# Kernel optimization log

Hardware: AMD Instinct MI355X
Metric: run time of the kernel (lower is better)

Reference implementation:

```python
import jax, jax.numpy as jnp
import numpy as np

WINDOW = 20  # window_size from init

def setup_inputs() -> dict:
    key = jax.random.key(0)
    ks = jax.random.split(key, 8)
    B, K, L, H = 8, 64, 1024, 256
    FFN = 3 * H * 4  # input_dim*ffn_ratio
    cand_span_reps = jax.random.normal(ks[0], (B, K, H), dtype=jnp.float32)
    token_reps = jax.random.normal(ks[1], (B, L, H), dtype=jnp.float32)
    W1 = jax.random.normal(ks[2], (3 * H, FFN), dtype=jnp.float32) * (1.0 / np.sqrt(3 * H))
    b1 = jnp.zeros((FFN,), dtype=jnp.float32)
    W2 = jax.random.normal(ks[3], (FFN, H), dtype=jnp.float32) * (1.0 / np.sqrt(FFN))
    b2 = jnp.zeros((H,), dtype=jnp.float32)
    cand_span_ids = jnp.sort(jax.random.randint(ks[4], (B, K, 2), 0, L), axis=-1)
    token_masks = jnp.ones((B, L), dtype=bool)
    return {"cand_span_reps": cand_span_reps, "token_reps": token_reps,
            "W1": W1, "b1": b1, "W2": W2, "b2": b2,
            "cand_span_ids": cand_span_ids, "token_masks": token_masks}

def _span_window_max(token_reps, span_ids, token_masks, window):
    # token_reps: [B,L,H]; span_ids: [B,K,2]; token_masks: [B,L]
    L = token_reps.shape[1]
    seq = jnp.arange(L)[None, None, :]                      # [1,1,L]
    start = span_ids[:, :, 0][:, :, None]                   # [B,K,1]
    end = span_ids[:, :, 1][:, :, None]                     # [B,K,1]
    mask = (((seq >= start - window) & (seq < start)) |
            ((seq > end) & (seq <= end + window)))
    mask = mask & token_masks[:, None, :]                   # [B,K,L]
    # masked max over L -> [B,K,H]
    filled = jnp.where(mask[..., None], token_reps[:, None, :, :], -jnp.inf)
    return jnp.max(filled, axis=2)

def reference(cand_span_reps, token_reps, W1, b1, W2, b2, cand_span_ids, token_masks):
    B, K, H = cand_span_reps.shape
    # Per-span pooled window context [B,K,H]. The pairwise context over the
    # UNION of head & tail windows equals the elementwise max of the two
    # per-span window maxes (max over A|B == max(max A, max B)).
    ctx = _span_window_max(token_reps, cand_span_ids, token_masks, WINDOW)
    context_reps = jnp.maximum(ctx[:, :, None, :], ctx[:, None, :, :])   # [B,K,K,H]
    head_reps = jnp.broadcast_to(cand_span_reps[:, :, None, :], (B, K, K, H))
    tail_reps = jnp.broadcast_to(cand_span_reps[:, None, :, :], (B, K, K, H))
    rel = jnp.concatenate([head_reps, tail_reps, context_reps], axis=-1)  # [B,K,K,3H]
    h = jax.nn.relu(jnp.einsum('bijd,df->bijf', rel, W1) + b1)
    out = jnp.einsum('bijf,fh->bijh', h, W2) + b2
    return out.reshape(B, K * K, H)
```

## Files before the change

kernel.cpp:

```cpp
#include <hip/hip_runtime.h>
#include <hip/hip_bf16.h>
#include <cstdint>
#include <cstddef>


typedef __attribute__((ext_vector_type(8))) short short8;
typedef __attribute__((ext_vector_type(4))) float f32x4;
typedef __attribute__((ext_vector_type(2))) unsigned int u32x2;

#define B_DIM 8
#define K_DIM 64
#define H_DIM 256
#define L_DIM 1024
#define FFN_DIM 3072
#define WINDOW 20

__device__ __forceinline__ unsigned short f2b(float f) {
  unsigned int u = __float_as_uint(f);
  unsigned int r = (u + 0x7FFFu + ((u >> 16) & 1u)) >> 16;
  return (unsigned short)r;
}
__device__ __forceinline__ float b2f(unsigned short h) {
  return __uint_as_float(((unsigned int)h) << 16);
}
__device__ __forceinline__ f32x4 zero4() {
  f32x4 z = {0.f, 0.f, 0.f, 0.f};
  return z;
}
__device__ __forceinline__ void gload_lds16(const void* g, void* l) {
  __builtin_amdgcn_global_load_lds(
      (const __attribute__((address_space(1))) void*)g,
      (__attribute__((address_space(3))) void*)l, 16, 0, 0);
}
__device__ __forceinline__ unsigned int cvt_pk_bf16(float lo, float hi) {
  unsigned int r;
  asm("v_cvt_pk_bf16_f32 %0, %1, %2" : "=v"(r) : "v"(lo), "v"(hi));
  return r;
}


__global__ void cvt_bf16_kernel(const float* __restrict__ in,
                                unsigned short* __restrict__ out, int n) {
  int i = blockIdx.x * blockDim.x + threadIdx.x;
  if (i < n) out[i] = f2b(in[i]);
}

__global__ void transpose_cvt_kernel(const float* __restrict__ in,
                                     unsigned short* __restrict__ out,
                                     int R, int C) {
  __shared__ float t[64][65];
  int c0 = blockIdx.x * 64, r0 = blockIdx.y * 64;
  int tr = threadIdx.x >> 6, tc = threadIdx.x & 63;
  for (int rr = tr; rr < 64; rr += 4)
    t[rr][tc] = in[(size_t)(r0 + rr) * C + (c0 + tc)];
  __syncthreads();
  for (int cc = tr; cc < 64; cc += 4)
    out[(size_t)(c0 + cc) * R + (r0 + tc)] = f2b(t[tc][cc]);
}

__global__ void ctx_kernel(const float* __restrict__ token,
                           const int* __restrict__ ids,
                           unsigned short* __restrict__ ctx) {
  int bk = blockIdx.x;
  int b = bk >> 6;
  int h = threadIdx.x;
  int s = ids[bk * 2 + 0];
  int e = ids[bk * 2 + 1];
  const float* tb = token + ((size_t)b * L_DIM) * H_DIM + h;
  float m = -INFINITY;
  int lo = s - WINDOW; if (lo < 0) lo = 0;
  for (int l2 = lo; l2 < s; ++l2) m = fmaxf(m, tb[(size_t)l2 * H_DIM]);
  int hi = e + WINDOW; if (hi > L_DIM - 1) hi = L_DIM - 1;
  for (int l2 = e + 1; l2 <= hi; ++l2) m = fmaxf(m, tb[(size_t)l2 * H_DIM]);
  ctx[(size_t)bk * H_DIM + h] = f2b(m);
}

__global__ __launch_bounds__(256) void at_gemm_kernel(
    const unsigned short* __restrict__ candb,
    const unsigned short* __restrict__ w1abt,
    const float* __restrict__ b1, float* __restrict__ AT) {
  int n0 = blockIdx.x * 64;
  int r0 = blockIdx.y * 64;
  __shared__ __align__(16) unsigned short A[64 * 256];
  int w = threadIdx.x >> 6, l = threadIdx.x & 63;
  int l15 = l & 15, l4 = l >> 4;
  {
    int row = w * 16 + l15;
    const short8* src = (const short8*)(candb + (size_t)(r0 + row) * H_DIM);
    #pragma unroll
    for (int t = 0; t < 8; ++t) {
      int u = l4 + 4 * t;
      short8 v = src[u];
      *(short8*)(A + row * 256 + ((u ^ (row & 7)) * 8)) = v;
    }
  }
  __syncthreads();
  f32x4 acc[4] = {zero4(), zero4(), zero4(), zero4()};
  int n = n0 + 16 * w + l15;
  const unsigned short* bp = w1abt + (size_t)n * H_DIM + l4 * 8;
  #pragma unroll
  for (int kk = 0; kk < 8; ++kk) {
    short8 bfrag = *(const short8*)(bp + kk * 32);
    #pragma unroll
    for (int rf = 0; rf < 4; ++rf) {
      int row = rf * 16 + l15;
      int u = kk * 4 + l4;
      short8 afrag = *(const short8*)(A + row * 256 + ((u ^ (row & 7)) * 8));
      acc[rf] = __builtin_amdgcn_mfma_f32_16x16x32_bf16(afrag, bfrag, acc[rf], 0, 0, 0);
    }
  }
  float bias = (n < FFN_DIM) ? b1[n] : 0.0f;
  #pragma unroll
  for (int rf = 0; rf < 4; ++rf) {
    #pragma unroll
    for (int qq = 0; qq < 4; ++qq) {
      int row = r0 + rf * 16 + l4 * 4 + qq;
      AT[(size_t)row * (2 * FFN_DIM) + n] = acc[rf][qq] + bias;
    }
  }
}

__global__ __launch_bounds__(512, 4) void fused_kernel(
    const unsigned short* __restrict__ ctx,
    const unsigned short* __restrict__ w1ct,
    const unsigned short* __restrict__ w2t,
    const float* __restrict__ AT,
    const float* __restrict__ b2,
    float* __restrict__ out) {
  int blk = blockIdx.x;
  blk = (blk & 7) * 64 + (blk >> 3);
  int b = blk >> 6, i = blk & 63;

  __shared__ __align__(16) char W1s[2 * 16384];
  __shared__ __align__(16) char W2s[2 * 16384];
  __shared__ __align__(16) char HcS[2 * 4096];

  int tid = threadIdx.x;
  int w = tid >> 6, l = tid & 63;
  int l15 = l & 15, l4 = l >> 4;
  int wl = l15 & 7;
  int s3 = (l15 >> 1) & 3;

  if (w < 4) {
    int wf = w & 1, wj2 = w >> 1;
    int jloc = 32 * wj2 + l15;

    short8 bfr[8][2];
    {
      const unsigned short* cb = ctx + ((size_t)b * K_DIM) * H_DIM;
      const unsigned short* ci = cb + (size_t)i * H_DIM;
      #pragma unroll
      for (int kk = 0; kk < 8; ++kk) {
        int hoff = kk * 32 + l4 * 8;
        short8 vi = *(const short8*)(ci + hoff);
        #pragma unroll
        for (int jb = 0; jb < 2; ++jb) {
          short8 vj = *(const short8*)(cb + (size_t)(jloc + jb * 16) * H_DIM + hoff);
          short8 vm;
          #pragma unroll
          for (int e = 0; e < 8; ++e) {
            float fa = b2f((unsigned short)vi[e]);
            float fb = b2f((unsigned short)vj[e]);
            vm[e] = (fa >= fb) ? vi[e] : vj[e];
          }
          bfr[kk][jb] = vm;
        }
      }
    }

    int tid_p = (w << 6) | l;
    int fr = tid_p >> 5, u32i = tid_p & 31;
    int offW1 = fr * 512 + (((u32i & 24) | ((u32i & 7) ^ (fr & 7))) << 4);
    auto stageW1 = [&](int c, int buf) {
      const char* g = (const char*)w1ct + (size_t)c * 16384 + offW1;
      char* d = &W1s[buf * 16384 + tid_p * 16];
      gload_lds16(g, d);
      gload_lds16(g + 4096, d + 4096);
      gload_lds16(g + 8192, d + 8192);
      gload_lds16(g + 12288, d + 12288);
    };

    int baseA = (16 * wf + l15) * 512;
    int offAe = (l4 ^ wl) << 4;
    int offAo = ((4 + l4) ^ wl) << 4;
    int uW = 2 * wf + (l4 >> 1);
    int offHw = jloc * 64 + ((uW ^ s3) << 4) + ((l4 & 1) << 3);

    const float* avp = AT + (size_t)(b * K_DIM + i) * (2 * FFN_DIM) + 16 * wf + 4 * l4;
    const float* tvp = AT + (size_t)(b * K_DIM + jloc) * (2 * FFN_DIM) + FFN_DIM + 16 * wf + 4 * l4;

    stageW1(0, 0);
    __builtin_amdgcn_sched_barrier(0);
    asm volatile("s_waitcnt vmcnt(0)" ::: "memory");
    __builtin_amdgcn_sched_barrier(0);
    __builtin_amdgcn_s_barrier();
    __builtin_amdgcn_sched_barrier(0);

    for (int c = 0; c <= 96; ++c) {
      f32x4 av = zero4(), tv0 = zero4(), tv1 = zero4();
      if (c < 96) {
        av  = *(const f32x4*)(avp + c * 32);
        tv0 = *(const f32x4*)(tvp + c * 32);
        tv1 = *(const f32x4*)(tvp + 16 * (2 * FFN_DIM) + c * 32);
      }
      __builtin_amdgcn_sched_barrier(0);
      if (c < 95) stageW1(c + 1, (c + 1) & 1);
      __builtin_amdgcn_sched_barrier(0);

      if (c < 96) {
        const char* w1p = &W1s[(c & 1) * 16384 + baseA];
        f32x4 acc1[2] = {zero4(), zero4()};
        __builtin_amdgcn_s_setprio(1);
        #pragma unroll
        for (int m = 0; m < 4; ++m) {
          short8 afe = *(const short8*)(w1p + m * 128 + offAe);
          acc1[0] = __builtin_amdgcn_mfma_f32_16x16x32_bf16(afe, bfr[2 * m][0], acc1[0], 0, 0, 0);
          acc1[1] = __builtin_amdgcn_mfma_f32_16x16x32_bf16(afe, bfr[2 * m][1], acc1[1], 0, 0, 0);
          short8 afo = *(const short8*)(w1p + m * 128 + offAo);
          acc1[0] = __builtin_amdgcn_mfma_f32_16x16x32_bf16(afo, bfr[2 * m + 1][0], acc1[0], 0, 0, 0);
          acc1[1] = __builtin_amdgcn_mfma_f32_16x16x32_bf16(afo, bfr[2 * m + 1][1], acc1[1], 0, 0, 0);
        }
        __builtin_amdgcn_s_setprio(0);

        char* hw = &HcS[(c & 1) * 4096];
        {
          float v0 = fmaxf(acc1[0][0] + av[0] + tv0[0], 0.0f);
          float v1 = fmaxf(acc1[0][1] + av[1] + tv0[1], 0.0f);
          float v2 = fmaxf(acc1[0][2] + av[2] + tv0[2], 0.0f);
          float v3 = fmaxf(acc1[0][3] + av[3] + tv0[3], 0.0f);
          u32x2 pk;
          pk.x = cvt_pk_bf16(v0, v1);
          pk.y = cvt_pk_bf16(v2, v3);
          *(u32x2*)(hw + offHw) = pk;
        }
        {
          float v0 = fmaxf(acc1[1][0] + av[0] + tv1[0], 0.0f);
          float v1 = fmaxf(acc1[1][1] + av[1] + tv1[1], 0.0f);
          float v2 = fmaxf(acc1[1][2] + av[2] + tv1[2], 0.0f);
          float v3 = fmaxf(acc1[1][3] + av[3] + tv1[3], 0.0f);
          u32x2 pk;
          pk.x = cvt_pk_bf16(v0, v1);
          pk.y = cvt_pk_bf16(v2, v3);
          *(u32x2*)(hw + offHw + 1024) = pk;
        }
      }

      __builtin_amdgcn_sched_barrier(0);
      asm volatile("s_waitcnt vmcnt(0) lgkmcnt(0)" ::: "memory");
      __builtin_amdgcn_sched_barrier(0);
      __builtin_amdgcn_s_barrier();
      __builtin_amdgcn_sched_barrier(0);
    }
  } else {
    int ch = w - 4;
    int tid_c = (ch << 6) | l;
    int h2 = tid_c >> 2, u2 = tid_c & 3;
    int offW2 = h2 * 6144 + ((u2 ^ ((h2 >> 1) & 3)) << 4);
    auto stageW2 = [&](int c, int buf) {
      const char* g = (const char*)w2t + (size_t)c * 64 + offW2;
      char* d = &W2s[buf * 16384 + tid_c * 16];
      gload_lds16(g, d);
      gload_lds16(g + 1 * 393216, d + 4096);
      gload_lds16(g + 2 * 393216, d + 8192);
      gload_lds16(g + 3 * 393216, d + 12288);
    };
    int baseW2 = ch * 4096 + l15 * 64 + ((l4 ^ s3) << 4);
    int baseHr = l15 * 64 + ((l4 ^ s3) << 4);

    f32x4 accO[4][4];
    #pragma unroll
    for (int cf = 0; cf < 4; ++cf)
      #pragma unroll
      for (int jt = 0; jt < 4; ++jt) accO[cf][jt] = zero4();

    __builtin_amdgcn_s_barrier();
    __builtin_amdgcn_sched_barrier(0);

    for (int c = 0; c <= 96; ++c) {
      if (c < 96) stageW2(c, c & 1);
      __builtin_amdgcn_sched_barrier(0);

      if (c > 0) {
        const char* w2p = &W2s[((c - 1) & 1) * 16384];
        const char* hcp = &HcS[((c - 1) & 1) * 4096];
        short8 wfr[4], hbv[4];
        #pragma unroll
        for (int cf = 0; cf < 4; ++cf)
          wfr[cf] = *(const short8*)(w2p + baseW2 + cf * 1024);
        #pragma unroll
        for (int jt = 0; jt < 4; ++jt)
          hbv[jt] = *(const short8*)(hcp + baseHr + jt * 1024);
        __builtin_amdgcn_s_setprio(1);
        #pragma unroll
        for (int cf = 0; cf < 4; ++cf)
          #pragma unroll
          for (int jt = 0; jt < 4; ++jt)
            accO[cf][jt] = __builtin_amdgcn_mfma_f32_16x16x32_bf16(wfr[cf], hbv[jt], accO[cf][jt], 0, 0, 0);
        __builtin_amdgcn_s_setprio(0);
      }

      __builtin_amdgcn_sched_barrier(0);
      asm volatile("s_waitcnt vmcnt(0) lgkmcnt(0)" ::: "memory");
      __builtin_amdgcn_sched_barrier(0);
      __builtin_amdgcn_s_barrier();
      __builtin_amdgcn_sched_barrier(0);
    }

    f32x4 bv[4];
    #pragma unroll
    for (int cf = 0; cf < 4; ++cf)
      bv[cf] = *(const f32x4*)(b2 + 64 * ch + cf * 16 + 4 * l4);
    #pragma unroll
    for (int jt = 0; jt < 4; ++jt) {
      int j = jt * 16 + l15;
      float* row = out + ((size_t)b * (K_DIM * K_DIM) + (size_t)i * K_DIM + j) * H_DIM;
      #pragma unroll
      for (int cf = 0; cf < 4; ++cf) {
        f32x4 v = accO[cf][jt] + bv[cf];
        *(f32x4*)(row + 64 * ch + cf * 16 + 4 * l4) = v;
      }
    }
  }
}


extern "C" void kernel_launch(void* const* d_in, const int* in_sizes, int n_in,
                              void* d_out, int out_size, void* d_ws, size_t ws_size,
                              hipStream_t stream) {
  const float* cand  = (const float*)d_in[0];
  const float* token = (const float*)d_in[1];
  const float* W1    = (const float*)d_in[2];
  const float* b1    = (const float*)d_in[3];
  const float* W2    = (const float*)d_in[4];
  const float* b2    = (const float*)d_in[5];
  const int*   ids   = (const int*)d_in[6];
  float* out = (float*)d_out;

  char* ws = (char*)d_ws;
  unsigned short* ctx   = (unsigned short*)(ws);
  unsigned short* candb = (unsigned short*)(ws + 262144);
  unsigned short* w1abt = (unsigned short*)(ws + 524288);
  unsigned short* w1ct  = (unsigned short*)(ws + 3670016);
  unsigned short* w2t   = (unsigned short*)(ws + 5242880);
  float*          AT    = (float*)(ws + 6815744);

  hipLaunchKernelGGL(cvt_bf16_kernel, dim3(512), dim3(256), 0, stream,
                     cand, candb, B_DIM * K_DIM * H_DIM);
  hipLaunchKernelGGL(transpose_cvt_kernel, dim3(48, 4), dim3(256), 0, stream,
                     W1, w1abt, 256, FFN_DIM);
  hipLaunchKernelGGL(transpose_cvt_kernel, dim3(48, 4), dim3(256), 0, stream,
                     W1 + (size_t)256 * FFN_DIM, w1abt + (size_t)FFN_DIM * 256, 256, FFN_DIM);
  hipLaunchKernelGGL(transpose_cvt_kernel, dim3(48, 4), dim3(256), 0, stream,
                     W1 + (size_t)512 * FFN_DIM, w1ct, 256, FFN_DIM);
  hipLaunchKernelGGL(transpose_cvt_kernel, dim3(4, 48), dim3(256), 0, stream,
                     W2, w2t, FFN_DIM, 256);
  hipLaunchKernelGGL(ctx_kernel, dim3(512), dim3(256), 0, stream, token, ids, ctx);
  hipLaunchKernelGGL(at_gemm_kernel, dim3(96, 8), dim3(256), 0, stream,
                     candb, w1abt, b1, AT);
  hipLaunchKernelGGL(fused_kernel, dim3(512), dim3(512), 0, stream,
                     ctx, w1ct, w2t, AT, b2, out);
}
```

Measured before the change: 185.6 us.

## Move W1 tile staging from producer waves to consumer waves

The W1 global-to-LDS staging loads move out of the first-GEMM waves into the second-GEMM waves, which now issue both the W1 and W2 async copies each iteration. The producer waves keep only their small bias-vector loads and MFMA work. Address arithmetic is also switched to incremented pointers instead of per-iteration offset recomputation. The aim is to free the critical-path producer waves from memory-issue work, at the cost of loading more onto the consumer waves and making the W1 prefetch depend on their timing relative to the barrier.

New measurement: 181.2 us. 1.02x faster.

```diff
diff --git a/kernel.cpp b/kernel.cpp
--- a/kernel.cpp
+++ b/kernel.cpp
@@ -168,46 +168,27 @@
       }
     }
 
-    int tid_p = (w << 6) | l;
-    int fr = tid_p >> 5, u32i = tid_p & 31;
-    int offW1 = fr * 512 + (((u32i & 24) | ((u32i & 7) ^ (fr & 7))) << 4);
-    auto stageW1 = [&](int c, int buf) {
-      const char* g = (const char*)w1ct + (size_t)c * 16384 + offW1;
-      char* d = &W1s[buf * 16384 + tid_p * 16];
-      gload_lds16(g, d);
-      gload_lds16(g + 4096, d + 4096);
-      gload_lds16(g + 8192, d + 8192);
-      gload_lds16(g + 12288, d + 12288);
-    };
-
     int baseA = (16 * wf + l15) * 512;
     int offAe = (l4 ^ wl) << 4;
     int offAo = ((4 + l4) ^ wl) << 4;
     int uW = 2 * wf + (l4 >> 1);
     int offHw = jloc * 64 + ((uW ^ s3) << 4) + ((l4 & 1) << 3);
 
-    const float* avp = AT + (size_t)(b * K_DIM + i) * (2 * FFN_DIM) + 16 * wf + 4 * l4;
-    const float* tvp = AT + (size_t)(b * K_DIM + jloc) * (2 * FFN_DIM) + FFN_DIM + 16 * wf + 4 * l4;
-
-    stageW1(0, 0);
-    __builtin_amdgcn_sched_barrier(0);
-    asm volatile("s_waitcnt vmcnt(0)" ::: "memory");
-    __builtin_amdgcn_sched_barrier(0);
+    const float* avp  = AT + (size_t)(b * K_DIM + i) * (2 * FFN_DIM) + 16 * wf + 4 * l4;
+    const float* tvp0 = AT + (size_t)(b * K_DIM + jloc) * (2 * FFN_DIM) + FFN_DIM + 16 * wf + 4 * l4;
+    const float* tvp1 = tvp0 + (size_t)16 * (2 * FFN_DIM);
+
     __builtin_amdgcn_s_barrier();
     __builtin_amdgcn_sched_barrier(0);
 
     for (int c = 0; c <= 96; ++c) {
-      f32x4 av = zero4(), tv0 = zero4(), tv1 = zero4();
       if (c < 96) {
-        av  = *(const f32x4*)(avp + c * 32);
-        tv0 = *(const f32x4*)(tvp + c * 32);
-        tv1 = *(const f32x4*)(tvp + 16 * (2 * FFN_DIM) + c * 32);
-      }
-      __builtin_amdgcn_sched_barrier(0);
-      if (c < 95) stageW1(c + 1, (c + 1) & 1);
-      __builtin_amdgcn_sched_barrier(0);
-
-      if (c < 96) {
+        f32x4 av  = *(const f32x4*)avp;
+        f32x4 tv0 = *(const f32x4*)tvp0;
+        f32x4 tv1 = *(const f32x4*)tvp1;
+        avp += 32; tvp0 += 32; tvp1 += 32;
+        __builtin_amdgcn_sched_barrier(0);
+
         const char* w1p = &W1s[(c & 1) * 16384 + baseA];
         f32x4 acc1[2] = {zero4(), zero4()};
         __builtin_amdgcn_s_setprio(1);
@@ -254,16 +235,17 @@
   } else {
     int ch = w - 4;
     int tid_c = (ch << 6) | l;
+
+    int fr = tid_c >> 5, u32i = tid_c & 31;
+    int offW1 = fr * 512 + (((u32i & 24) | ((u32i & 7) ^ (fr & 7))) << 4);
     int h2 = tid_c >> 2, u2 = tid_c & 3;
     int offW2 = h2 * 6144 + ((u2 ^ ((h2 >> 1) & 3)) << 4);
-    auto stageW2 = [&](int c, int buf) {
-      const char* g = (const char*)w2t + (size_t)c * 64 + offW2;
-      char* d = &W2s[buf * 16384 + tid_c * 16];
-      gload_lds16(g, d);
-      gload_lds16(g + 1 * 393216, d + 4096);
-      gload_lds16(g + 2 * 393216, d + 8192);
-      gload_lds16(g + 3 * 393216, d + 12288);
-    };
+
+    const char* gW1 = (const char*)w1ct + offW1;
+    const char* gW2 = (const char*)w2t + offW2;
+    char* dW1base = &W1s[tid_c * 16];
+    char* dW2base = &W2s[tid_c * 16];
+
     int baseW2 = ch * 4096 + l15 * 64 + ((l4 ^ s3) << 4);
     int baseHr = l15 * 64 + ((l4 ^ s3) << 4);
 
@@ -273,11 +255,36 @@
       #pragma unroll
       for (int jt = 0; jt < 4; ++jt) accO[cf][jt] = zero4();
 
+    {
+      gload_lds16(gW1, dW1base);
+      gload_lds16(gW1 + 4096, dW1base + 4096);
+      gload_lds16(gW1 + 8192, dW1base + 8192);
+      gload_lds16(gW1 + 12288, dW1base + 12288);
+      gW1 += 16384;
+    }
+    __builtin_amdgcn_sched_barrier(0);
+    asm volatile("s_waitcnt vmcnt(0)" ::: "memory");
+    __builtin_amdgcn_sched_barrier(0);
     __builtin_amdgcn_s_barrier();
     __builtin_amdgcn_sched_barrier(0);
 
     for (int c = 0; c <= 96; ++c) {
-      if (c < 96) stageW2(c, c & 1);
+      if (c < 95) {
+        char* d = dW1base + ((c + 1) & 1) * 16384;
+        gload_lds16(gW1, d);
+        gload_lds16(gW1 + 4096, d + 4096);
+        gload_lds16(gW1 + 8192, d + 8192);
+        gload_lds16(gW1 + 12288, d + 12288);
+        gW1 += 16384;
+      }
+      if (c < 96) {
+        char* d = dW2base + (c & 1) * 16384;
+        gload_lds16(gW2, d);
+        gload_lds16(gW2 + 1 * 393216, d + 4096);
+        gload_lds16(gW2 + 2 * 393216, d + 8192);
+        gload_lds16(gW2 + 3 * 393216, d + 12288);
+        gW2 += 64;
+      }
       __builtin_amdgcn_sched_barrier(0);
 
       if (c > 0) {
```
